# Kernel tuning notes

Hardware: AMD Instinct MI355X
Metric: run time of the kernel (lower is better)

## Reference

```python
import jax, jax.numpy as jnp
import numpy as np

DIM = 1024
NUM_EXPERTS = 8
TOP_K = 2
B, S = 2, 2048
HID = 4 * DIM


def setup_inputs() -> dict:
    key = jax.random.key(0)
    ks = jax.random.split(key, 7)
    scale = 0.02
    x = jax.random.normal(ks[0], (B, S, DIM), dtype=jnp.float32)
    gate_w = jax.random.normal(ks[1], (DIM, NUM_EXPERTS), dtype=jnp.float32) * scale
    gate_b = jnp.zeros((NUM_EXPERTS,), dtype=jnp.float32)
    w1 = jax.random.normal(ks[2], (NUM_EXPERTS, DIM, HID), dtype=jnp.float32) * scale
    b1 = jnp.zeros((NUM_EXPERTS, HID), dtype=jnp.float32)
    w2 = jax.random.normal(ks[3], (NUM_EXPERTS, HID, DIM), dtype=jnp.float32) * scale
    b2 = jnp.zeros((NUM_EXPERTS, DIM), dtype=jnp.float32)
    return {"x": x, "gate_w": gate_w, "gate_b": gate_b,
            "w1": w1, "b1": b1, "w2": w2, "b2": b2}


def reference(x, gate_w, gate_b, w1, b1, w2, b2):
    # Gate: [B,S,E]
    gates = jnp.einsum('bsd,de->bse', x, gate_w) + gate_b
    top_w, top_idx = jax.lax.top_k(gates, TOP_K)          # [B,S,K]
    probs = jax.nn.softmax(top_w, axis=-1)                # softmax over selected logits
    # Dense all-expert FFN (matches original: every expert runs on every token)
    h = jnp.einsum('bsd,edh->bseh', x, w1) + b1           # [B,S,E,4D]
    h = jax.nn.gelu(h, approximate=False)                 # exact GELU (torch default)
    y = jnp.einsum('bseh,ehd->bsed', h, w2) + b2          # [B,S,E,D]
    # Select top-k experts per token and combine
    sel = jnp.take_along_axis(y, top_idx[..., None], axis=2)   # [B,S,K,D]
    return jnp.sum(sel * probs[..., None], axis=2)        # [B,S,D]
```

## Files before the change

### kernel.cpp

```cpp
#include <hip/hip_runtime.h>
#include <hip/hip_bf16.h>

#define T_TOKENS 4096
#define DIM      1024
#define HID      4096
#define NE       8
#define CAP      4096
#define SPLITS   4
#define KSP      (HID / SPLITS)

typedef __attribute__((ext_vector_type(8))) short  bf16x8;
typedef __attribute__((ext_vector_type(4))) float  f32x4;
typedef __attribute__((ext_vector_type(4))) ushort u16x4;

__device__ static inline ushort f2bf(float f) {
    __hip_bfloat16 h = __float2bfloat16(f);
    return *(ushort*)&h;
}

__device__ static inline void gll16(const void* g, void* l) {
    __builtin_amdgcn_global_load_lds(
        (const __attribute__((address_space(1))) void*)g,
        (__attribute__((address_space(3))) void*)l,
        16, 0, 0);
}

__global__ __launch_bounds__(64) void gate_kernel(
    const float* __restrict__ x, const float* __restrict__ gw,
    const float* __restrict__ gb, __hip_bfloat16* __restrict__ xb,
    int* __restrict__ counts, int* __restrict__ tlist, float* __restrict__ plist)
{
    const int tok = blockIdx.x;
    const int l   = threadIdx.x;
    const float* xr = x + (size_t)tok * DIM;

    float part[NE];
#pragma unroll
    for (int e = 0; e < NE; e++) part[e] = 0.f;

#pragma unroll
    for (int i = 0; i < DIM / 64; i++) {
        int d = i * 64 + l;
        float xv = xr[d];
        xb[(size_t)tok * DIM + d] = __float2bfloat16(xv);
        const float4* g4 = (const float4*)(gw + (size_t)d * NE);
        float4 a = g4[0], b = g4[1];
        part[0] += xv * a.x; part[1] += xv * a.y;
        part[2] += xv * a.z; part[3] += xv * a.w;
        part[4] += xv * b.x; part[5] += xv * b.y;
        part[6] += xv * b.z; part[7] += xv * b.w;
    }
#pragma unroll
    for (int off = 32; off > 0; off >>= 1) {
#pragma unroll
        for (int e = 0; e < NE; e++) part[e] += __shfl_xor(part[e], off, 64);
    }
    if (l == 0) {
        float lg[NE];
#pragma unroll
        for (int e = 0; e < NE; e++) lg[e] = part[e] + gb[e];
        int i0 = 0;
#pragma unroll
        for (int e = 1; e < NE; e++) if (lg[e] > lg[i0]) i0 = e;
        int i1 = (i0 == 0) ? 1 : 0;
#pragma unroll
        for (int e = 0; e < NE; e++) if (e != i0 && lg[e] > lg[i1]) i1 = e;
        float t  = expf(lg[i1] - lg[i0]);
        float p0 = 1.f / (1.f + t);
        float p1 = t / (1.f + t);
        int pos0 = atomicAdd(&counts[i0], 1);
        tlist[i0 * CAP + pos0] = tok; plist[i0 * CAP + pos0] = p0;
        int pos1 = atomicAdd(&counts[i1], 1);
        tlist[i1 * CAP + pos1] = tok; plist[i1 * CAP + pos1] = p1;
    }
}

__global__ void finalize_kernel(const int* __restrict__ counts, int* __restrict__ base)
{
    if (threadIdx.x == 0) {
        int acc = 0;
        for (int e = 0; e < NE; e++) { base[e] = acc; acc += counts[e]; }
        base[NE] = acc;
    }
}

__global__ __launch_bounds__(256) void transpose_cvt64(
    const float* __restrict__ in, __hip_bfloat16* __restrict__ outp, int K, int N)
{
    __shared__ ushort tile[64][68];
    const int e  = blockIdx.z;
    const float* src = in + (size_t)e * K * N;
    ushort* dst = (ushort*)outp + (size_t)e * K * N;
    const int k0 = blockIdx.y * 64, n0 = blockIdx.x * 64;
    const int tid = threadIdx.x;

    const int rn4 = (tid & 15) * 4;
    const int rk  = tid >> 4;
#pragma unroll
    for (int p = 0; p < 4; p++) {
        int k = rk + p * 16;
        float4 v = *(const float4*)&src[(size_t)(k0 + k) * N + n0 + rn4];
        tile[k][rn4 + 0] = f2bf(v.x);
        tile[k][rn4 + 1] = f2bf(v.y);
        tile[k][rn4 + 2] = f2bf(v.z);
        tile[k][rn4 + 3] = f2bf(v.w);
    }
    __syncthreads();
    const int wk4 = (tid & 15) * 4;
    const int wn  = tid >> 4;
#pragma unroll
    for (int p = 0; p < 4; p++) {
        int n = wn + p * 16;
        u16x4 u;
        u[0] = tile[wk4 + 0][n];
        u[1] = tile[wk4 + 1][n];
        u[2] = tile[wk4 + 2][n];
        u[3] = tile[wk4 + 3][n];
        *(u16x4*)&dst[(size_t)(n0 + n) * K + k0 + wk4] = u;
    }
}

__global__ __launch_bounds__(256, 3) void ffn1_kernel(
    const __hip_bfloat16* __restrict__ xb, const __hip_bfloat16* __restrict__ w1t,
    const float* __restrict__ b1, const int* __restrict__ counts,
    const int* __restrict__ base, const int* __restrict__ tlist,
    __hip_bfloat16* __restrict__ H)
{
    const int e  = blockIdx.z;
    const int ne = counts[e];
    const int rb = blockIdx.y, cb = blockIdx.x;
    if (rb * 128 >= ne) return;

    __shared__ __align__(16) ushort ldsA[2][4096];
    __shared__ __align__(16) ushort ldsB[2][4096];

    const int t = threadIdx.x;
    const int l = t & 63, w = t >> 6;
    const int wr = w >> 1, wc = w & 1;

    const int slot0 = w * 128 + l;
    const int slot1 = w * 128 + 64 + l;
    const int row0 = slot0 >> 2, row1 = slot1 >> 2;
    const int ch0 = ((slot0 & 3) ^ ((row0 >> 1) & 3)) * 8;
    const int ch1 = ((slot1 & 3) ^ ((row1 >> 1) & 3)) * 8;
    const int lo0 = w * 1024;
    const int lo1 = w * 1024 + 512;

    const int r0g = rb * 128 + row0, r1g = rb * 128 + row1;
    const int tok0 = tlist[e * CAP + (r0g < ne ? r0g : 0)];
    const int tok1 = tlist[e * CAP + (r1g < ne ? r1g : 0)];
    const ushort* aS0 = (const ushort*)xb + (size_t)tok0 * DIM + ch0;
    const ushort* aS1 = (const ushort*)xb + (size_t)tok1 * DIM + ch1;
    const ushort* bS0 = (const ushort*)w1t + ((size_t)e * HID + cb * 128 + row0) * DIM + ch0;
    const ushort* bS1 = (const ushort*)w1t + ((size_t)e * HID + cb * 128 + row1) * DIM + ch1;

    f32x4 acc[4][4];
#pragma unroll
    for (int i = 0; i < 4; i++)
#pragma unroll
        for (int j = 0; j < 4; j++) acc[i][j] = (f32x4){0.f, 0.f, 0.f, 0.f};

    const int lm = l & 15, lgp = l >> 4;
    const int rch = (lgp ^ ((lm >> 1) & 3)) * 8;

    gll16(aS0, &ldsA[0][lo0]); gll16(aS1, &ldsA[0][lo1]);
    gll16(bS0, &ldsB[0][lo0]); gll16(bS1, &ldsB[0][lo1]);

    int cur = 0;
    const int NK = DIM / 32;
    for (int ks = 0; ks < NK; ks++) {
        __syncthreads();
        if (ks + 1 < NK) {
            const int ko = (ks + 1) * 32;
            gll16(aS0 + ko, &ldsA[cur ^ 1][lo0]); gll16(aS1 + ko, &ldsA[cur ^ 1][lo1]);
            gll16(bS0 + ko, &ldsB[cur ^ 1][lo0]); gll16(bS1 + ko, &ldsB[cur ^ 1][lo1]);
        }
        bf16x8 af[4], bfr[4];
#pragma unroll
        for (int i = 0; i < 4; i++) {
            int row = wr * 64 + i * 16 + lm;
            af[i] = *(const bf16x8*)&ldsA[cur][row * 32 + rch];
        }
#pragma unroll
        for (int j = 0; j < 4; j++) {
            int row = wc * 64 + j * 16 + lm;
            bfr[j] = *(const bf16x8*)&ldsB[cur][row * 32 + rch];
        }
#pragma unroll
        for (int i = 0; i < 4; i++)
#pragma unroll
            for (int j = 0; j < 4; j++)
                acc[i][j] = __builtin_amdgcn_mfma_f32_16x16x32_bf16(af[i], bfr[j], acc[i][j], 0, 0, 0);
        cur ^= 1;
    }

    const int hb = base[e];
#pragma unroll
    for (int i = 0; i < 4; i++) {
#pragma unroll
        for (int jj = 0; jj < 4; jj++) {
            int r = rb * 128 + wr * 64 + i * 16 + lgp * 4 + jj;
            if (r < ne) {
                size_t hrow = (size_t)(hb + r) * HID;
#pragma unroll
                for (int j = 0; j < 4; j++) {
                    int col = cb * 128 + wc * 64 + j * 16 + lm;
                    float v = acc[i][j][jj] + b1[e * HID + col];
                    v = 0.5f * v * (1.0f + erff(v * 0.70710678118654752f));
                    H[hrow + col] = __float2bfloat16(v);
                }
            }
        }
    }
}

__global__ __launch_bounds__(256, 3) void ffn2_kernel(
    const __hip_bfloat16* __restrict__ H, const __hip_bfloat16* __restrict__ w2t,
    const float* __restrict__ b2, const int* __restrict__ counts,
    const int* __restrict__ base, const int* __restrict__ tlist,
    const float* __restrict__ plist, float* __restrict__ out)
{
    const int e  = blockIdx.z;
    const int ne = counts[e];
    const int rb = blockIdx.y >> 2;
    const int sp = blockIdx.y & 3;
    const int cb = blockIdx.x;
    if (rb * 128 >= ne) return;

    __shared__ __align__(16) ushort ldsA[2][4096];
    __shared__ __align__(16) ushort ldsB[2][4096];

    const int t = threadIdx.x;
    const int l = t & 63, w = t >> 6;
    const int wr = w >> 1, wc = w & 1;

    const int slot0 = w * 128 + l;
    const int slot1 = w * 128 + 64 + l;
    const int row0 = slot0 >> 2, row1 = slot1 >> 2;
    const int ch0 = ((slot0 & 3) ^ ((row0 >> 1) & 3)) * 8;
    const int ch1 = ((slot1 & 3) ^ ((row1 >> 1) & 3)) * 8;
    const int lo0 = w * 1024;
    const int lo1 = w * 1024 + 512;

    const int hb = base[e];
    const int r0g = rb * 128 + row0, r1g = rb * 128 + row1;
    const int hr0 = hb + (r0g < ne ? r0g : ne - 1);
    const int hr1 = hb + (r1g < ne ? r1g : ne - 1);
    const size_t ko0 = (size_t)sp * KSP;
    const ushort* aS0 = (const ushort*)H + (size_t)hr0 * HID + ko0 + ch0;
    const ushort* aS1 = (const ushort*)H + (size_t)hr1 * HID + ko0 + ch1;
    const ushort* bS0 = (const ushort*)w2t + ((size_t)e * DIM + cb * 128 + row0) * HID + ko0 + ch0;
    const ushort* bS1 = (const ushort*)w2t + ((size_t)e * DIM + cb * 128 + row1) * HID + ko0 + ch1;

    f32x4 acc[4][4];
#pragma unroll
    for (int i = 0; i < 4; i++)
#pragma unroll
        for (int j = 0; j < 4; j++) acc[i][j] = (f32x4){0.f, 0.f, 0.f, 0.f};

    const int lm = l & 15, lgp = l >> 4;
    const int rch = (lgp ^ ((lm >> 1) & 3)) * 8;

    gll16(aS0, &ldsA[0][lo0]); gll16(aS1, &ldsA[0][lo1]);
    gll16(bS0, &ldsB[0][lo0]); gll16(bS1, &ldsB[0][lo1]);

    int cur = 0;
    const int NK = KSP / 32;
    for (int ks = 0; ks < NK; ks++) {
        __syncthreads();
        if (ks + 1 < NK) {
            const int ko = (ks + 1) * 32;
            gll16(aS0 + ko, &ldsA[cur ^ 1][lo0]); gll16(aS1 + ko, &ldsA[cur ^ 1][lo1]);
            gll16(bS0 + ko, &ldsB[cur ^ 1][lo0]); gll16(bS1 + ko, &ldsB[cur ^ 1][lo1]);
        }
        bf16x8 af[4], bfr[4];
#pragma unroll
        for (int i = 0; i < 4; i++) {
            int row = wr * 64 + i * 16 + lm;
            af[i] = *(const bf16x8*)&ldsA[cur][row * 32 + rch];
        }
#pragma unroll
        for (int j = 0; j < 4; j++) {
            int row = wc * 64 + j * 16 + lm;
            bfr[j] = *(const bf16x8*)&ldsB[cur][row * 32 + rch];
        }
#pragma unroll
        for (int i = 0; i < 4; i++)
#pragma unroll
            for (int j = 0; j < 4; j++)
                acc[i][j] = __builtin_amdgcn_mfma_f32_16x16x32_bf16(af[i], bfr[j], acc[i][j], 0, 0, 0);
        cur ^= 1;
    }

#pragma unroll
    for (int i = 0; i < 4; i++) {
#pragma unroll
        for (int jj = 0; jj < 4; jj++) {
            int r = rb * 128 + wr * 64 + i * 16 + lgp * 4 + jj;
            if (r < ne) {
                int tok  = tlist[e * CAP + r];
                float p  = plist[e * CAP + r];
                float* orow = out + (size_t)tok * DIM;
#pragma unroll
                for (int j = 0; j < 4; j++) {
                    int col = cb * 128 + wc * 64 + j * 16 + lm;
                    float v = acc[i][j][jj];
                    if (sp == 0) v += b2[e * DIM + col];
                    unsafeAtomicAdd(&orow[col], v * p);
                }
            }
        }
    }
}

extern "C" void kernel_launch(void* const* d_in, const int* in_sizes, int n_in,
                              void* d_out, int out_size, void* d_ws, size_t ws_size,
                              hipStream_t stream)
{
    const float* x  = (const float*)d_in[0];
    const float* gw = (const float*)d_in[1];
    const float* gb = (const float*)d_in[2];
    const float* w1 = (const float*)d_in[3];
    const float* b1 = (const float*)d_in[4];
    const float* w2 = (const float*)d_in[5];
    const float* b2 = (const float*)d_in[6];
    float* out = (float*)d_out;

    char* ws = (char*)d_ws;
    __hip_bfloat16* w1t = (__hip_bfloat16*)(ws);
    __hip_bfloat16* w2t = (__hip_bfloat16*)(ws + 67108864);
    __hip_bfloat16* Hb  = (__hip_bfloat16*)(ws + 134217728);
    __hip_bfloat16* xb  = (__hip_bfloat16*)(ws + 201326592);
    int*   tlist  = (int*)  (ws + 209715200);
    float* plist  = (float*)(ws + 209846272);
    int*   counts = (int*)  (ws + 209977344);
    int*   basep  = (int*)  (ws + 209977408);

    hipMemsetAsync(out, 0, (size_t)T_TOKENS * DIM * sizeof(float), stream);
    hipMemsetAsync(counts, 0, 64, stream);

    gate_kernel<<<T_TOKENS, 64, 0, stream>>>(x, gw, gb, xb, counts, tlist, plist);
    finalize_kernel<<<1, 64, 0, stream>>>(counts, basep);

    transpose_cvt64<<<dim3(HID / 64, DIM / 64, NE), 256, 0, stream>>>(w1, w1t, DIM, HID);
    transpose_cvt64<<<dim3(DIM / 64, HID / 64, NE), 256, 0, stream>>>(w2, w2t, HID, DIM);

    ffn1_kernel<<<dim3(HID / 128, CAP / 128, NE), 256, 0, stream>>>(
        xb, w1t, b1, counts, basep, tlist, Hb);
    ffn2_kernel<<<dim3(DIM / 128, (CAP / 128) * SPLITS, NE), 256, 0, stream>>>(
        Hb, w2t, b2, counts, basep, tlist, plist, out);
}
```

Measured before the change: 540.8 us.

## Triple-buffer LDS with explicit vmcnt waits and halve FFN2 split-K

Both GEMM kernels move from a double-buffered LDS pipeline with __syncthreads to a three-stage ring buffer. Two k-tiles are prefetched ahead, and explicit s_waitcnt vmcnt(4) plus a raw s_barrier let one tile's loads stay in flight while another is computed. FFN2 also drops from 4 to 2 split-K partitions, which halves the atomic-add traffic into the output and doubles the K loop per block. LDS per block rises from 32KB to 48KB, which may reduce occupancy against the launch_bounds(256,3) target. If the host grid still assumes SPLITS=4 blocks in y, FFN2's indexing would be inconsistent.

```diff
diff --git a/kernel.cpp b/kernel.cpp
--- a/kernel.cpp
+++ b/kernel.cpp
@@ -6,7 +6,7 @@
 #define HID      4096
 #define NE       8
 #define CAP      4096
-#define SPLITS   4
+#define SPLITS   2
 #define KSP      (HID / SPLITS)
 
 typedef __attribute__((ext_vector_type(8))) short  bf16x8;
@@ -131,8 +131,8 @@
     const int rb = blockIdx.y, cb = blockIdx.x;
     if (rb * 128 >= ne) return;
 
-    __shared__ __align__(16) ushort ldsA[2][4096];
-    __shared__ __align__(16) ushort ldsB[2][4096];
+    __shared__ __align__(16) ushort ldsA[3][4096];
+    __shared__ __align__(16) ushort ldsB[3][4096];
 
     const int t = threadIdx.x;
     const int l = t & 63, w = t >> 6;
@@ -163,35 +163,43 @@
     const int lm = l & 15, lgp = l >> 4;
     const int rch = (lgp ^ ((lm >> 1) & 3)) * 8;
 
+    const int NK = DIM / 32;
     gll16(aS0, &ldsA[0][lo0]); gll16(aS1, &ldsA[0][lo1]);
     gll16(bS0, &ldsB[0][lo0]); gll16(bS1, &ldsB[0][lo1]);
-
-    int cur = 0;
-    const int NK = DIM / 32;
+    gll16(aS0 + 32, &ldsA[1][lo0]); gll16(aS1 + 32, &ldsA[1][lo1]);
+    gll16(bS0 + 32, &ldsB[1][lo0]); gll16(bS1 + 32, &ldsB[1][lo1]);
+
+    int rbuf = 0, wbuf = 2;
+#pragma unroll 1
     for (int ks = 0; ks < NK; ks++) {
-        __syncthreads();
-        if (ks + 1 < NK) {
-            const int ko = (ks + 1) * 32;
-            gll16(aS0 + ko, &ldsA[cur ^ 1][lo0]); gll16(aS1 + ko, &ldsA[cur ^ 1][lo1]);
-            gll16(bS0 + ko, &ldsB[cur ^ 1][lo0]); gll16(bS1 + ko, &ldsB[cur ^ 1][lo1]);
-        }
+        if (ks < NK - 1) { asm volatile("s_waitcnt vmcnt(4)" ::: "memory"); }
+        else             { asm volatile("s_waitcnt vmcnt(0)" ::: "memory"); }
+        __builtin_amdgcn_s_barrier();
+        if (ks + 2 < NK) {
+            const int ko = (ks + 2) * 32;
+            gll16(aS0 + ko, &ldsA[wbuf][lo0]); gll16(aS1 + ko, &ldsA[wbuf][lo1]);
+            gll16(bS0 + ko, &ldsB[wbuf][lo0]); gll16(bS1 + ko, &ldsB[wbuf][lo1]);
+        }
+        const ushort* pA = &ldsA[rbuf][0];
+        const ushort* pB = &ldsB[rbuf][0];
         bf16x8 af[4], bfr[4];
 #pragma unroll
         for (int i = 0; i < 4; i++) {
             int row = wr * 64 + i * 16 + lm;
-            af[i] = *(const bf16x8*)&ldsA[cur][row * 32 + rch];
+            af[i] = *(const bf16x8*)&pA[row * 32 + rch];
         }
 #pragma unroll
         for (int j = 0; j < 4; j++) {
             int row = wc * 64 + j * 16 + lm;
-            bfr[j] = *(const bf16x8*)&ldsB[cur][row * 32 + rch];
+            bfr[j] = *(const bf16x8*)&pB[row * 32 + rch];
         }
 #pragma unroll
         for (int i = 0; i < 4; i++)
 #pragma unroll
             for (int j = 0; j < 4; j++)
                 acc[i][j] = __builtin_amdgcn_mfma_f32_16x16x32_bf16(af[i], bfr[j], acc[i][j], 0, 0, 0);
-        cur ^= 1;
+        rbuf = (rbuf == 2) ? 0 : rbuf + 1;
+        wbuf = (wbuf == 2) ? 0 : wbuf + 1;
     }
 
     const int hb = base[e];
@@ -222,13 +230,13 @@
 {
     const int e  = blockIdx.z;
     const int ne = counts[e];
-    const int rb = blockIdx.y >> 2;
-    const int sp = blockIdx.y & 3;
+    const int rb = blockIdx.y >> 1;
+    const int sp = blockIdx.y & 1;
     const int cb = blockIdx.x;
     if (rb * 128 >= ne) return;
 
-    __shared__ __align__(16) ushort ldsA[2][4096];
-    __shared__ __align__(16) ushort ldsB[2][4096];
+    __shared__ __align__(16) ushort ldsA[3][4096];
+    __shared__ __align__(16) ushort ldsB[3][4096];
 
     const int t = threadIdx.x;
     const int l = t & 63, w = t >> 6;
@@ -261,35 +269,43 @@
     const int lm = l & 15, lgp = l >> 4;
     const int rch = (lgp ^ ((lm >> 1) & 3)) * 8;
 
+    const int NK = KSP / 32;
     gll16(aS0, &ldsA[0][lo0]); gll16(aS1, &ldsA[0][lo1]);
     gll16(bS0, &ldsB[0][lo0]); gll16(bS1, &ldsB[0][lo1]);
-
-    int cur = 0;
-    const int NK = KSP / 32;
+    gll16(aS0 + 32, &ldsA[1][lo0]); gll16(aS1 + 32, &ldsA[1][lo1]);
+    gll16(bS0 + 32, &ldsB[1][lo0]); gll16(bS1 + 32, &ldsB[1][lo1]);
+
+    int rbuf = 0, wbuf = 2;
+#pragma unroll 1
     for (int ks = 0; ks < NK; ks++) {
-        __syncthreads();
-        if (ks + 1 < NK) {
-            const int ko = (ks + 1) * 32;
-            gll16(aS0 + ko, &ldsA[cur ^ 1][lo0]); gll16(aS1 + ko, &ldsA[cur ^ 1][lo1]);
-            gll16(bS0 + ko, &ldsB[cur ^ 1][lo0]); gll16(bS1 + ko, &ldsB[cur ^ 1][lo1]);
-        }
+        if (ks < NK - 1) { asm volatile("s_waitcnt vmcnt(4)" ::: "memory"); }
+        else             { asm volatile("s_waitcnt vmcnt(0)" ::: "memory"); }
+        __builtin_amdgcn_s_barrier();
+        if (ks + 2 < NK) {
+            const int ko = (ks + 2) * 32;
+            gll16(aS0 + ko, &ldsA[wbuf][lo0]); gll16(aS1 + ko, &ldsA[wbuf][lo1]);
+            gll16(bS0 + ko, &ldsB[wbuf][lo0]); gll16(bS1 + ko, &ldsB[wbuf][lo1]);
+        }
+        const ushort* pA = &ldsA[rbuf][0];
+        const ushort* pB = &ldsB[rbuf][0];
         bf16x8 af[4], bfr[4];
 #pragma unroll
         for (int i = 0; i < 4; i++) {
             int row = wr * 64 + i * 16 + lm;
-            af[i] = *(const bf16x8*)&ldsA[cur][row * 32 + rch];
+            af[i] = *(const bf16x8*)&pA[row * 32 + rch];
         }
 #pragma unroll
         for (int j = 0; j < 4; j++) {
             int row = wc * 64 + j * 16 + lm;
-            bfr[j] = *(const bf16x8*)&ldsB[cur][row * 32 + rch];
+            bfr[j] = *(const bf16x8*)&pB[row * 32 + rch];
         }
 #pragma unroll
         for (int i = 0; i < 4; i++)
 #pragma unroll
             for (int j = 0; j < 4; j++)
                 acc[i][j] = __builtin_amdgcn_mfma_f32_16x16x32_bf16(af[i], bfr[j], acc[i][j], 0, 0, 0);
-        cur ^= 1;
+        rbuf = (rbuf == 2) ? 0 : rbuf + 1;
+        wbuf = (wbuf == 2) ? 0 : wbuf + 1;
     }
 
 #pragma unroll
```

Result: faster. 503.6 us (-6.9%).

## Enlarge expert GEMM tiles to 256x256 with 8 waves and deeper LDS pipeline

Applied to the files above, without the earlier changes.

Both expert FFN GEMMs move from 128x128 tiles with 4 waves to 256x256 tiles with 8 waves. They use a 128KB LDS buffer with a four-stage load pipeline, explicit vmcnt waits, barrier-interleaved MFMA clusters and setprio. The ffn2 split-K drops from 4 to 2 to match, which halves the atomic output traffic. The goal is more operand reuse per loaded byte and better overlap of global loads with MFMA. The cost is higher register and LDS pressure, lower occupancy, and fewer blocks for small expert counts.

```diff
diff --git a/kernel.cpp b/kernel.cpp
--- a/kernel.cpp
+++ b/kernel.cpp
@@ -6,7 +6,7 @@
 #define HID      4096
 #define NE       8
 #define CAP      4096
-#define SPLITS   4
+#define SPLITS   2
 #define KSP      (HID / SPLITS)
 
 typedef __attribute__((ext_vector_type(8))) short  bf16x8;
@@ -24,6 +24,8 @@
         (__attribute__((address_space(3))) void*)l,
         16, 0, 0);
 }
+
+#define MFMA16(a, b, c) __builtin_amdgcn_mfma_f32_16x16x32_bf16((a), (b), (c), 0, 0, 0)
 
 __global__ __launch_bounds__(64) void gate_kernel(
     const float* __restrict__ x, const float* __restrict__ gw,
@@ -120,7 +122,114 @@
     }
 }
 
-__global__ __launch_bounds__(256, 3) void ffn1_kernel(
+
+#define AOFFc(d,s) (((d)*2+(s))*8192)
+#define BOFFc(d,s) (32768 + ((d)*2+(s))*8192)
+
+#define MFMA_CL(nj0, nj1)                                                    \
+    _Pragma("unroll")                                                        \
+    for (int mi = 0; mi < 8; mi++) {                                         \
+        acc[mi][nj0] = MFMA16(af[mi], bf##nj0, acc[mi][nj0]);                \
+        acc[mi][nj1] = MFMA16(af[mi], bf##nj1, acc[mi][nj1]);                \
+    }
+
+#define GEMM_CORE(NT, srcA0, srcA1, srcB0, srcB1)                            \
+    f32x4 acc[8][4];                                                         \
+    _Pragma("unroll")                                                        \
+    for (int i = 0; i < 8; i++)                                              \
+        _Pragma("unroll")                                                    \
+        for (int j = 0; j < 4; j++) acc[i][j] = (f32x4){0.f,0.f,0.f,0.f};    \
+    const int lm = l & 15, kg = l >> 4;                                      \
+    const int rch = (kg ^ ((lm >> 1) & 3)) * 8;                              \
+    const int a0 = (wr * 128 + lm) * 32 + rch;                               \
+    const int b0 = (wc * 64 + lm) * 32 + rch;                                \
+                \
+    gll16(srcA0,      &lds[AOFFc(0,0) + w*512]);                             \
+    gll16(srcA1,      &lds[AOFFc(0,0) + 4096 + w*512]);                      \
+    gll16(srcB0,      &lds[BOFFc(0,0) + w*512]);                             \
+    gll16(srcB1,      &lds[BOFFc(0,0) + 4096 + w*512]);                      \
+    gll16(srcA0 + 32, &lds[AOFFc(0,1) + w*512]);                             \
+    gll16(srcA1 + 32, &lds[AOFFc(0,1) + 4096 + w*512]);                      \
+    gll16(srcB0 + 32, &lds[BOFFc(0,1) + w*512]);                             \
+    gll16(srcB1 + 32, &lds[BOFFc(0,1) + 4096 + w*512]);                      \
+    asm volatile("s_waitcnt vmcnt(4)" ::: "memory");                         \
+    gll16(srcA0 + 64, &lds[AOFFc(1,0) + w*512]);                             \
+    gll16(srcA1 + 64, &lds[AOFFc(1,0) + 4096 + w*512]);                      \
+    gll16(srcB0 + 64, &lds[BOFFc(1,0) + w*512]);                             \
+    gll16(srcB1 + 64, &lds[BOFFc(1,0) + 4096 + w*512]);                      \
+    gll16(srcA0 + 96, &lds[AOFFc(1,1) + w*512]);                             \
+    gll16(srcA1 + 96, &lds[AOFFc(1,1) + 4096 + w*512]);                      \
+    asm volatile("s_waitcnt vmcnt(6)" ::: "memory");                         \
+    __builtin_amdgcn_s_barrier();                                            \
+    _Pragma("unroll 1")                                                      \
+    for (int t = 0; t < NT; t++) {                                           \
+        const int d   = t & 1;                                               \
+        const int aof  = d * 16384,        bof  = 32768 + d * 16384;         \
+        const int aofN = (d^1) * 16384,    bofN = 32768 + (d^1) * 16384;     \
+        bf16x8 af[8]; bf16x8 bf0, bf1, bf2, bf3;                             \
+                \
+        _Pragma("unroll")                                                    \
+        for (int mi = 0; mi < 8; mi++)                                       \
+            af[mi] = *(const bf16x8*)&lds[aof + a0 + mi*512];                \
+        bf0 = *(const bf16x8*)&lds[bof + b0];                                \
+        bf1 = *(const bf16x8*)&lds[bof + b0 + 512];                          \
+        if (t + 1 < NT) {                                                    \
+            size_t ko = (size_t)(t+1)*64 + 32;                               \
+            gll16(srcB0 + ko, &lds[bofN + 8192 + w*512]);                    \
+            gll16(srcB1 + ko, &lds[bofN + 8192 + 4096 + w*512]);             \
+        }                                                                    \
+        __builtin_amdgcn_s_barrier();                                        \
+        __builtin_amdgcn_s_setprio(1);                                       \
+        MFMA_CL(0, 1)                                                        \
+        __builtin_amdgcn_s_setprio(0);                                       \
+        __builtin_amdgcn_s_barrier();                                        \
+                          \
+        bf2 = *(const bf16x8*)&lds[bof + b0 + 1024];                         \
+        bf3 = *(const bf16x8*)&lds[bof + b0 + 1536];                         \
+        if (t + 2 < NT) {                                                    \
+            size_t ko = (size_t)(t+2)*64;                                    \
+            gll16(srcA0 + ko, &lds[aof + w*512]);                            \
+            gll16(srcA1 + ko, &lds[aof + 4096 + w*512]);                     \
+        }                                                                    \
+        __builtin_amdgcn_s_barrier();                                        \
+        __builtin_amdgcn_s_setprio(1);                                       \
+        MFMA_CL(2, 3)                                                        \
+        __builtin_amdgcn_s_setprio(0);                                       \
+        __builtin_amdgcn_s_barrier();                                        \
+                \
+        _Pragma("unroll")                                                    \
+        for (int mi = 0; mi < 8; mi++)                                       \
+            af[mi] = *(const bf16x8*)&lds[aof + 8192 + a0 + mi*512];         \
+        bf0 = *(const bf16x8*)&lds[bof + 8192 + b0];                         \
+        bf1 = *(const bf16x8*)&lds[bof + 8192 + b0 + 512];                   \
+        if (t + 2 < NT) {                                                    \
+            size_t ko = (size_t)(t+2)*64;                                    \
+            gll16(srcB0 + ko, &lds[bof + w*512]);                            \
+            gll16(srcB1 + ko, &lds[bof + 4096 + w*512]);                     \
+        }                                                                    \
+        __builtin_amdgcn_s_barrier();                                        \
+        __builtin_amdgcn_s_setprio(1);                                       \
+        MFMA_CL(0, 1)                                                        \
+        __builtin_amdgcn_s_setprio(0);                                       \
+        __builtin_amdgcn_s_barrier();                                        \
+            \
+        bf2 = *(const bf16x8*)&lds[bof + 8192 + b0 + 1024];                  \
+        bf3 = *(const bf16x8*)&lds[bof + 8192 + b0 + 1536];                  \
+        if (t + 2 < NT) {                                                    \
+            size_t ko = (size_t)(t+2)*64 + 32;                               \
+            gll16(srcA0 + ko, &lds[aof + 8192 + w*512]);                     \
+            gll16(srcA1 + ko, &lds[aof + 8192 + 4096 + w*512]);              \
+        }                                                                    \
+        __builtin_amdgcn_s_barrier();                                        \
+        __builtin_amdgcn_s_setprio(1);                                       \
+        MFMA_CL(2, 3)                                                        \
+        __builtin_amdgcn_s_setprio(0);                                       \
+        if (t < NT - 2) { asm volatile("s_waitcnt vmcnt(6)" ::: "memory"); } \
+        else            { asm volatile("s_waitcnt vmcnt(0)" ::: "memory"); } \
+        __builtin_amdgcn_s_barrier();                                        \
+    }
+
+__global__ __launch_bounds__(512, 2) void ffn1_kernel(
     const __hip_bfloat16* __restrict__ xb, const __hip_bfloat16* __restrict__ w1t,
     const float* __restrict__ b1, const int* __restrict__ counts,
     const int* __restrict__ base, const int* __restrict__ tlist,
@@ -129,92 +238,49 @@
     const int e  = blockIdx.z;
     const int ne = counts[e];
     const int rb = blockIdx.y, cb = blockIdx.x;
-    if (rb * 128 >= ne) return;
-
-    __shared__ __align__(16) ushort ldsA[2][4096];
-    __shared__ __align__(16) ushort ldsB[2][4096];
-
-    const int t = threadIdx.x;
-    const int l = t & 63, w = t >> 6;
-    const int wr = w >> 1, wc = w & 1;
-
-    const int slot0 = w * 128 + l;
-    const int slot1 = w * 128 + 64 + l;
-    const int row0 = slot0 >> 2, row1 = slot1 >> 2;
-    const int ch0 = ((slot0 & 3) ^ ((row0 >> 1) & 3)) * 8;
-    const int ch1 = ((slot1 & 3) ^ ((row1 >> 1) & 3)) * 8;
-    const int lo0 = w * 1024;
-    const int lo1 = w * 1024 + 512;
-
-    const int r0g = rb * 128 + row0, r1g = rb * 128 + row1;
-    const int tok0 = tlist[e * CAP + (r0g < ne ? r0g : 0)];
-    const int tok1 = tlist[e * CAP + (r1g < ne ? r1g : 0)];
-    const ushort* aS0 = (const ushort*)xb + (size_t)tok0 * DIM + ch0;
-    const ushort* aS1 = (const ushort*)xb + (size_t)tok1 * DIM + ch1;
-    const ushort* bS0 = (const ushort*)w1t + ((size_t)e * HID + cb * 128 + row0) * DIM + ch0;
-    const ushort* bS1 = (const ushort*)w1t + ((size_t)e * HID + cb * 128 + row1) * DIM + ch1;
-
-    f32x4 acc[4][4];
-#pragma unroll
-    for (int i = 0; i < 4; i++)
-#pragma unroll
-        for (int j = 0; j < 4; j++) acc[i][j] = (f32x4){0.f, 0.f, 0.f, 0.f};
-
-    const int lm = l & 15, lgp = l >> 4;
-    const int rch = (lgp ^ ((lm >> 1) & 3)) * 8;
-
-    gll16(aS0, &ldsA[0][lo0]); gll16(aS1, &ldsA[0][lo1]);
-    gll16(bS0, &ldsB[0][lo0]); gll16(bS1, &ldsB[0][lo1]);
-
-    int cur = 0;
-    const int NK = DIM / 32;
-    for (int ks = 0; ks < NK; ks++) {
-        __syncthreads();
-        if (ks + 1 < NK) {
-            const int ko = (ks + 1) * 32;
-            gll16(aS0 + ko, &ldsA[cur ^ 1][lo0]); gll16(aS1 + ko, &ldsA[cur ^ 1][lo1]);
-            gll16(bS0 + ko, &ldsB[cur ^ 1][lo0]); gll16(bS1 + ko, &ldsB[cur ^ 1][lo1]);
-        }
-        bf16x8 af[4], bfr[4];
-#pragma unroll
-        for (int i = 0; i < 4; i++) {
-            int row = wr * 64 + i * 16 + lm;
-            af[i] = *(const bf16x8*)&ldsA[cur][row * 32 + rch];
-        }
-#pragma unroll
-        for (int j = 0; j < 4; j++) {
-            int row = wc * 64 + j * 16 + lm;
-            bfr[j] = *(const bf16x8*)&ldsB[cur][row * 32 + rch];
-        }
-#pragma unroll
-        for (int i = 0; i < 4; i++)
-#pragma unroll
-            for (int j = 0; j < 4; j++)
-                acc[i][j] = __builtin_amdgcn_mfma_f32_16x16x32_bf16(af[i], bfr[j], acc[i][j], 0, 0, 0);
-        cur ^= 1;
-    }
+    if (rb * 256 >= ne) return;
+
+    __shared__ __align__(16) ushort lds[65536];
+
+    const int tid = threadIdx.x;
+    const int l = tid & 63, w = tid >> 6;
+    const int wr = w >> 2, wc = w & 3;
+
+    const int srow = tid >> 2;
+    const int sch  = tid & 3;
+    const int sc0  = (sch ^ ((srow >> 1) & 3)) * 8;
+    const int rA0g = rb * 256 + srow;
+    const int rA1g = rA0g + 128;
+    const int tok0 = tlist[e * CAP + (rA0g < ne ? rA0g : ne - 1)];
+    const int tok1 = tlist[e * CAP + (rA1g < ne ? rA1g : ne - 1)];
+    const ushort* srcA0 = (const ushort*)xb + (size_t)tok0 * DIM + sc0;
+    const ushort* srcA1 = (const ushort*)xb + (size_t)tok1 * DIM + sc0;
+    const ushort* srcB0 = (const ushort*)w1t + ((size_t)e * HID + cb * 256 + srow) * DIM + sc0;
+    const ushort* srcB1 = srcB0 + (size_t)128 * DIM;
+
+    GEMM_CORE(16, srcA0, srcA1, srcB0, srcB1)
 
     const int hb = base[e];
 #pragma unroll
-    for (int i = 0; i < 4; i++) {
-#pragma unroll
-        for (int jj = 0; jj < 4; jj++) {
-            int r = rb * 128 + wr * 64 + i * 16 + lgp * 4 + jj;
-            if (r < ne) {
-                size_t hrow = (size_t)(hb + r) * HID;
-#pragma unroll
-                for (int j = 0; j < 4; j++) {
-                    int col = cb * 128 + wc * 64 + j * 16 + lm;
-                    float v = acc[i][j][jj] + b1[e * HID + col];
+    for (int nj = 0; nj < 4; nj++) {
+        int col = cb * 256 + wc * 64 + nj * 16 + lm;
+        float bias = b1[e * HID + col];
+#pragma unroll
+        for (int mi = 0; mi < 8; mi++) {
+#pragma unroll
+            for (int jj = 0; jj < 4; jj++) {
+                int r = rb * 256 + wr * 128 + mi * 16 + kg * 4 + jj;
+                if (r < ne) {
+                    float v = acc[mi][nj][jj] + bias;
                     v = 0.5f * v * (1.0f + erff(v * 0.70710678118654752f));
-                    H[hrow + col] = __float2bfloat16(v);
+                    H[(size_t)(hb + r) * HID + col] = __float2bfloat16(v);
                 }
             }
         }
     }
 }
 
-__global__ __launch_bounds__(256, 3) void ffn2_kernel(
+__global__ __launch_bounds__(512, 2) void ffn2_kernel(
     const __hip_bfloat16* __restrict__ H, const __hip_bfloat16* __restrict__ w2t,
     const float* __restrict__ b2, const int* __restrict__ counts,
     const int* __restrict__ base, const int* __restrict__ tlist,
@@ -222,89 +288,46 @@
 {
     const int e  = blockIdx.z;
     const int ne = counts[e];
-    const int rb = blockIdx.y >> 2;
-    const int sp = blockIdx.y & 3;
+    const int rb = blockIdx.y >> 1;
+    const int sp = blockIdx.y & 1;
     const int cb = blockIdx.x;
-    if (rb * 128 >= ne) return;
-
-    __shared__ __align__(16) ushort ldsA[2][4096];
-    __shared__ __align__(16) ushort ldsB[2][4096];
-
-    const int t = threadIdx.x;
-    const int l = t & 63, w = t >> 6;
-    const int wr = w >> 1, wc = w & 1;
-
-    const int slot0 = w * 128 + l;
-    const int slot1 = w * 128 + 64 + l;
-    const int row0 = slot0 >> 2, row1 = slot1 >> 2;
-    const int ch0 = ((slot0 & 3) ^ ((row0 >> 1) & 3)) * 8;
-    const int ch1 = ((slot1 & 3) ^ ((row1 >> 1) & 3)) * 8;
-    const int lo0 = w * 1024;
-    const int lo1 = w * 1024 + 512;
-
-    const int hb = base[e];
-    const int r0g = rb * 128 + row0, r1g = rb * 128 + row1;
-    const int hr0 = hb + (r0g < ne ? r0g : ne - 1);
-    const int hr1 = hb + (r1g < ne ? r1g : ne - 1);
+    if (rb * 256 >= ne) return;
+
+    __shared__ __align__(16) ushort lds[65536];
+
+    const int tid = threadIdx.x;
+    const int l = tid & 63, w = tid >> 6;
+    const int wr = w >> 2, wc = w & 3;
+
+    const int srow = tid >> 2;
+    const int sch  = tid & 3;
+    const int sc0  = (sch ^ ((srow >> 1) & 3)) * 8;
+    const int hb   = base[e];
+    const int rA0g = rb * 256 + srow;
+    const int rA1g = rA0g + 128;
+    const int hr0  = hb + (rA0g < ne ? rA0g : ne - 1);
+    const int hr1  = hb + (rA1g < ne ? rA1g : ne - 1);
     const size_t ko0 = (size_t)sp * KSP;
-    const ushort* aS0 = (const ushort*)H + (size_t)hr0 * HID + ko0 + ch0;
-    const ushort* aS1 = (const ushort*)H + (size_t)hr1 * HID + ko0 + ch1;
-    const ushort* bS0 = (const ushort*)w2t + ((size_t)e * DIM + cb * 128 + row0) * HID + ko0 + ch0;
-    const ushort* bS1 = (const ushort*)w2t + ((size_t)e * DIM + cb * 128 + row1) * HID + ko0 + ch1;
-
-    f32x4 acc[4][4];
-#pragma unroll
-    for (int i = 0; i < 4; i++)
-#pragma unroll
-        for (int j = 0; j < 4; j++) acc[i][j] = (f32x4){0.f, 0.f, 0.f, 0.f};
-
-    const int lm = l & 15, lgp = l >> 4;
-    const int rch = (lgp ^ ((lm >> 1) & 3)) * 8;
-
-    gll16(aS0, &ldsA[0][lo0]); gll16(aS1, &ldsA[0][lo1]);
-    gll16(bS0, &ldsB[0][lo0]); gll16(bS1, &ldsB[0][lo1]);
-
-    int cur = 0;
-    const int NK = KSP / 32;
-    for (int ks = 0; ks < NK; ks++) {
-        __syncthreads();
-        if (ks + 1 < NK) {
-            const int ko = (ks + 1) * 32;
-            gll16(aS0 + ko, &ldsA[cur ^ 1][lo0]); gll16(aS1 + ko, &ldsA[cur ^ 1][lo1]);
-            gll16(bS0 + ko, &ldsB[cur ^ 1][lo0]); gll16(bS1 + ko, &ldsB[cur ^ 1][lo1]);
-        }
-        bf16x8 af[4], bfr[4];
-#pragma unroll
-        for (int i = 0; i < 4; i++) {
-            int row = wr * 64 + i * 16 + lm;
-            af[i] = *(const bf16x8*)&ldsA[cur][row * 32 + rch];
-        }
-#pragma unroll
-        for (int j = 0; j < 4; j++) {
-            int row = wc * 64 + j * 16 + lm;
-            bfr[j] = *(const bf16x8*)&ldsB[cur][row * 32 + rch];
-        }
-#pragma unroll
-        for (int i = 0; i < 4; i++)
-#pragma unroll
-            for (int j = 0; j < 4; j++)
-                acc[i][j] = __builtin_amdgcn_mfma_f32_16x16x32_bf16(af[i], bfr[j], acc[i][j], 0, 0, 0);
-        cur ^= 1;
-    }
-
-#pragma unroll
-    for (int i = 0; i < 4; i++) {
+    const ushort* srcA0 = (const ushort*)H + (size_t)hr0 * HID + ko0 + sc0;
+    const ushort* srcA1 = (const ushort*)H + (size_t)hr1 * HID + ko0 + sc0;
+    const ushort* srcB0 = (const ushort*)w2t + ((size_t)e * DIM + cb * 256 + srow) * HID + ko0 + sc0;
+    const ushort* srcB1 = srcB0 + (size_t)128 * HID;
+
+    GEMM_CORE(32, srcA0, srcA1, srcB0, srcB1)
+
+#pragma unroll
+    for (int mi = 0; mi < 8; mi++) {
 #pragma unroll
         for (int jj = 0; jj < 4; jj++) {
-            int r = rb * 128 + wr * 64 + i * 16 + lgp * 4 + jj;
+            int r = rb * 256 + wr * 128 + mi * 16 + kg * 4 + jj;
             if (r < ne) {
-                int tok  = tlist[e * CAP + r];
-                float p  = plist[e * CAP + r];
+                int tok = tlist[e * CAP + r];
+                float p = plist[e * CAP + r];
                 float* orow = out + (size_t)tok * DIM;
 #pragma unroll
-                for (int j = 0; j < 4; j++) {
-                    int col = cb * 128 + wc * 64 + j * 16 + lm;
-                    float v = acc[i][j][jj];
+                for (int nj = 0; nj < 4; nj++) {
+                    int col = cb * 256 + wc * 64 + nj * 16 + lm;
+                    float v = acc[mi][nj][jj];
                     if (sp == 0) v += b2[e * DIM + col];
                     unsafeAtomicAdd(&orow[col], v * p);
                 }
@@ -345,8 +368,8 @@
     transpose_cvt64<<<dim3(HID / 64, DIM / 64, NE), 256, 0, stream>>>(w1, w1t, DIM, HID);
     transpose_cvt64<<<dim3(DIM / 64, HID / 64, NE), 256, 0, stream>>>(w2, w2t, HID, DIM);
 
-    ffn1_kernel<<<dim3(HID / 128, CAP / 128, NE), 256, 0, stream>>>(
+    ffn1_kernel<<<dim3(HID / 256, CAP / 256, NE), 512, 0, stream>>>(
         xb, w1t, b1, counts, basep, tlist, Hb);
-    ffn2_kernel<<<dim3(DIM / 128, (CAP / 128) * SPLITS, NE), 256, 0, stream>>>(
+    ffn2_kernel<<<dim3(DIM / 256, (CAP / 256) * SPLITS, NE), 512, 0, stream>>>(
         Hb, w2t, b2, counts, basep, tlist, plist, out);
 }
```

After: 543.1 us. Within noise of the previous version (+0.4%).
